# Performance work log

Hardware: AMD Instinct MI355X
Metric: run time of the kernel (lower is better)

## Reference

```python
import jax, jax.numpy as jnp
import numpy as np
from jax import lax

D_MODEL = 1024
N_HEADS = 16
HEAD_DIM = D_MODEL // N_HEADS
B, S = 4, 2048
EPS = 1e-5


def setup_inputs() -> dict:
    key = jax.random.key(0)
    ks = jax.random.split(key, 8)
    sc = 1.0 / np.sqrt(D_MODEL)
    return {
        "x": jax.random.normal(ks[0], (B, S, D_MODEL), dtype=jnp.float32),
        "Wq": jax.random.normal(ks[1], (D_MODEL, D_MODEL), dtype=jnp.float32) * sc,
        "Wk": jax.random.normal(ks[2], (D_MODEL, D_MODEL), dtype=jnp.float32) * sc,
        "Wv": jax.random.normal(ks[3], (D_MODEL, D_MODEL), dtype=jnp.float32) * sc,
        "Wa": jax.random.normal(ks[4], (D_MODEL, N_HEADS), dtype=jnp.float32) * sc,
        "ba": jnp.zeros((N_HEADS,), dtype=jnp.float32),
        "Wb": jax.random.normal(ks[5], (D_MODEL, N_HEADS), dtype=jnp.float32) * sc,
        "bb": jnp.zeros((N_HEADS,), dtype=jnp.float32),
        "Wg": jax.random.normal(ks[6], (D_MODEL, D_MODEL), dtype=jnp.float32) * sc,
        "Wo": jax.random.normal(ks[7], (D_MODEL, D_MODEL), dtype=jnp.float32) * sc,
        "g_norm": jnp.ones((D_MODEL,), dtype=jnp.float32),
    }


def _l2_normalize(v, eps=1e-12):
    # F.normalize(dim=-1) in float32
    v32 = v.astype(jnp.float32)
    n = jnp.sqrt(jnp.sum(v32 * v32, axis=-1, keepdims=True))
    return (v32 / jnp.maximum(n, eps)).astype(v.dtype)


def _rmsnorm(x, w):
    x32 = x.astype(jnp.float32)
    rms = lax.rsqrt(jnp.mean(x32 * x32, axis=-1, keepdims=True) + EPS)
    return (x32 * rms).astype(x.dtype) * w


def reference(x, Wq, Wk, Wv, Wa, ba, Wb, bb, Wg, Wo, g_norm):
    batch, seq_len, d_model = x.shape
    H, hd = N_HEADS, HEAD_DIM
    residual_input = x

    # projections -> [B, S, H, hd]
    q = (x @ Wq).reshape(batch, seq_len, H, hd)
    k = (x @ Wk).reshape(batch, seq_len, H, hd)
    v = (x @ Wv).reshape(batch, seq_len, H, hd)
    q = _l2_normalize(q)
    k = _l2_normalize(k)

    alpha = jax.nn.sigmoid(x @ Wa + ba)  # [B, S, H]
    beta = jax.nn.sigmoid(x @ Wb + bb)   # [B, S, H]

    # time-major for scan: [S, B, H, ...]
    qt = jnp.moveaxis(q, 1, 0)
    kt = jnp.moveaxis(k, 1, 0)
    vt = jnp.moveaxis(v, 1, 0)
    at = jnp.moveaxis(alpha, 1, 0)
    bt = jnp.moveaxis(beta, 1, 0)

    state0 = jnp.zeros((batch, H, hd, hd), dtype=x.dtype)

    def step(state, inp):
        q_t, k_t, v_t, a_t, b_t = inp  # [B,H,hd], [B,H]
        pred = jnp.einsum('bhde,bhd->bhe', state, k_t)
        error = v_t - pred
        update = jnp.einsum('bhe,bhd->bhde', b_t[..., None] * error, k_t)
        state = a_t[..., None, None] * state + update
        out = jnp.einsum('bhde,bhd->bhe', state, q_t)
        return state, out

    _, ys = lax.scan(step, state0, (qt, kt, vt, at, bt))  # ys: [S,B,H,hd]
    y = jnp.moveaxis(ys, 0, 1).reshape(batch, seq_len, d_model)

    gate = jax.nn.silu(residual_input @ Wg)
    y = _rmsnorm(y, g_norm) * gate
    return y @ Wo


if __name__ == "__main__":
    out = reference(**setup_inputs())
    print(out.shape)
```

## Files before the change

### kernel.cpp

```cpp
#include <hip/hip_runtime.h>
#include <hip/hip_bf16.h>
#include <math.h>

typedef __attribute__((ext_vector_type(8))) short bf16x8s;
typedef __attribute__((ext_vector_type(4))) float f32x4;

#define SEQ 2048
#define NTOK 8192
#define NQKV 3200

static __device__ __forceinline__ float bf2f(unsigned short u) {
  union { unsigned int i; float f; } c; c.i = ((unsigned int)u) << 16; return c.f;
}
static __device__ __forceinline__ unsigned short f2bf(float f) {
  union { float f; unsigned int i; } c; c.f = f;
  unsigned int x = c.i;
  return (unsigned short)((x + 0x7FFFu + ((x >> 16) & 1u)) >> 16);
}

static __device__ __forceinline__ float red16(float x) {
  union { float f; int i; } c, d;
  c.f = x; d.i = __builtin_amdgcn_update_dpp(0, c.i, 0xB1, 0xF, 0xF, true); x += d.f;
  c.f = x; d.i = __builtin_amdgcn_update_dpp(0, c.i, 0x4E, 0xF, 0xF, true); x += d.f;
  c.f = x; d.i = __builtin_amdgcn_update_dpp(0, c.i, 0x141, 0xF, 0xF, true); x += d.f;
  c.f = x; d.i = __builtin_amdgcn_update_dpp(0, c.i, 0x140, 0xF, 0xF, true); x += d.f;
  return x;
}

__global__ __launch_bounds__(256) void castx_k(const float* __restrict__ in,
                                               unsigned short* __restrict__ out, int n4) {
  int i = blockIdx.x * 256 + threadIdx.x;
  if (i >= n4) return;
  float4 v = ((const float4*)in)[i];
  ushort4 o;
  o.x = f2bf(v.x); o.y = f2bf(v.y); o.z = f2bf(v.z); o.w = f2bf(v.w);
  ((ushort4*)out)[i] = o;
}

__global__ void transpose_k(const float* __restrict__ in,
                            unsigned short* __restrict__ out, int R, int C) {
  __shared__ unsigned short tile[32][33];
  int c0 = blockIdx.x * 32, r0 = blockIdx.y * 32;
  int tx = threadIdx.x, ty = threadIdx.y;
  for (int i = ty; i < 32; i += 8)
    tile[i][tx] = f2bf(in[(size_t)(r0 + i) * C + c0 + tx]);
  __syncthreads();
  for (int i = ty; i < 32; i += 8)
    out[(size_t)(c0 + i) * R + r0 + tx] = tile[tx][i];
}

__global__ void build_wabT(const float* __restrict__ Wa,
                           const float* __restrict__ Wb,
                           unsigned short* __restrict__ rows) {
  int i = blockIdx.x * 256 + threadIdx.x;
  int j = i >> 10, k = i & 1023;
  float v = 0.f;
  if (j < 16) v = Wa[k * 16 + j];
  else if (j < 32) v = Wb[k * 16 + (j - 16)];
  rows[(size_t)j * 1024 + k] = f2bf(v);
}

template<int MODE>
__global__ __launch_bounds__(256) void gemm_bt(const unsigned short* __restrict__ A,
                                               const unsigned short* __restrict__ Bt,
                                               void* __restrict__ Cv,
                                               int M, int N, int K,
                                               const float* __restrict__ ba,
                                               const float* __restrict__ bbp,
                                               float* __restrict__ alphaF,
                                               float* __restrict__ betaF) {
  __shared__ __align__(16) unsigned short As[128 * 32];
  __shared__ __align__(16) unsigned short Bs[128 * 32];
  int tiles_n = N >> 7;
  int tm = blockIdx.x / tiles_n, tn = blockIdx.x % tiles_n;
  int m0 = tm << 7, n0 = tn << 7;
  int tid = threadIdx.x;
  int wave = tid >> 6, lane = tid & 63;
  int wm = wave >> 1, wn = wave & 1;
  int r = lane & 15, qd = lane >> 4;
  int lr = lane >> 2, lc = lane & 3;

  f32x4 acc[4][4];
#pragma unroll
  for (int mi = 0; mi < 4; mi++)
#pragma unroll
    for (int ni = 0; ni < 4; ni++) acc[mi][ni] = (f32x4){0.f, 0.f, 0.f, 0.f};

  for (int k0 = 0; k0 < K; k0 += 32) {
#pragma unroll
    for (int gi = 0; gi < 2; ++gi) {
      int g = wave + gi * 4;
      int row = g * 16 + lr;
      const unsigned short* ga = A + (size_t)(m0 + row) * K + k0 + lc * 8;
      const unsigned short* gb = Bt + (size_t)(n0 + row) * K + k0 + lc * 8;
      __builtin_amdgcn_global_load_lds(
          (const __attribute__((address_space(1))) unsigned int*)ga,
          (__attribute__((address_space(3))) unsigned int*)(As + g * 512 + lane * 8),
          16, 0, 0);
      __builtin_amdgcn_global_load_lds(
          (const __attribute__((address_space(1))) unsigned int*)gb,
          (__attribute__((address_space(3))) unsigned int*)(Bs + g * 512 + lane * 8),
          16, 0, 0);
    }
    __syncthreads();
    bf16x8s af[4], bfr[4];
#pragma unroll
    for (int mi = 0; mi < 4; mi++)
      af[mi] = *(const bf16x8s*)&As[(wm * 64 + mi * 16 + r) * 32 + qd * 8];
#pragma unroll
    for (int ni = 0; ni < 4; ni++)
      bfr[ni] = *(const bf16x8s*)&Bs[(wn * 64 + ni * 16 + r) * 32 + qd * 8];
#pragma unroll
    for (int mi = 0; mi < 4; mi++)
#pragma unroll
      for (int ni = 0; ni < 4; ni++)
        acc[mi][ni] = __builtin_amdgcn_mfma_f32_16x16x32_bf16(af[mi], bfr[ni], acc[mi][ni], 0, 0, 0);
    __syncthreads();
  }

  bool qk = (MODE == 2) && (n0 < 2048);
#pragma unroll
  for (int mi = 0; mi < 4; mi++) {
    f32x4 sc = (f32x4){1.f, 1.f, 1.f, 1.f};
    if (qk) {
      f32x4 ss = acc[mi][0] * acc[mi][0] + acc[mi][1] * acc[mi][1]
               + acc[mi][2] * acc[mi][2] + acc[mi][3] * acc[mi][3];
#pragma unroll
      for (int cc = 0; cc < 4; cc++) {
        float s = red16(ss[cc]);
        sc[cc] = 1.f / fmaxf(sqrtf(s), 1e-12f);
      }
    }
#pragma unroll
    for (int ni = 0; ni < 4; ni++)
#pragma unroll
      for (int reg = 0; reg < 4; reg++) {
        int m = m0 + wm * 64 + mi * 16 + qd * 4 + reg;
        int n = n0 + wn * 64 + ni * 16 + r;
        float a = acc[mi][ni][reg];
        if (MODE == 0) ((unsigned short*)Cv)[(size_t)m * N + n] = f2bf(a);
        else if (MODE == 1) ((float*)Cv)[(size_t)m * N + n] = a;
        else {
          if (qk) a *= sc[reg];
          if (n < 3072) ((unsigned short*)Cv)[(size_t)m * 3072 + n] = f2bf(a);
          else if (n < 3104) {
            int j = n - 3072;
            float bias = (j < 16) ? ba[j] : bbp[j - 16];
            float s = 1.f / (1.f + expf(-(a + bias)));
            if (j < 16) alphaF[(size_t)m * 16 + j] = s;
            else        betaF[(size_t)m * 16 + (j - 16)] = s;
          }
        }
      }
  }
}

#define D_OFF_STHI 0
#define D_OFF_STLO 8192
#define D_OFF_K    16384
#define D_OFF_Q    24576
#define D_OFF_V    32768
#define D_OFF_KT   40960
#define D_OFF_MT   45056
#define D_OFF_GBF  53248
#define D_OFF_CTHI 57344
#define D_OFF_CTLO 67584
#define D_OFF_W    77824
#define D_OFF_U    86016
#define D_OFF_AB   102400
#define D_LDS_SIZE 104512

static __device__ __forceinline__ float rdlane(float v, int i) {
  return __int_as_float(__builtin_amdgcn_readlane(__float_as_int(v), i));
}

__global__ __launch_bounds__(512, 2) void dscan_k(const unsigned short* __restrict__ qkv,
                                                  const float* __restrict__ alphaF,
                                                  const float* __restrict__ betaF,
                                                  unsigned short* __restrict__ y) {
  extern __shared__ char smem[];
  const int bh = blockIdx.x;
  const int b = bh >> 4, h = bh & 15;
  const int tid = threadIdx.x, wid = tid >> 6, lane = tid & 63;
  const int r = lane & 15, qd = lane >> 4;

  float* abf = (float*)(smem + D_OFF_AB);

  auto stage_jobs = [&](int cn) {
    int buf = cn & 1;
    int tok0 = b * SEQ + cn * 32;
    int row = lane >> 3, s8 = lane & 7;
    int sx = ((s8 ^ (row & 7)) * 8);
    {
      int p = (wid < 4) ? wid : wid - 4;
      int colbase = (wid < 4) ? (1024 + h * 64) : (h * 64);
      int off = (wid < 4) ? D_OFF_K : D_OFF_Q;
      const unsigned short* src = qkv + (size_t)(tok0 + p * 8 + row) * 3072 + colbase + sx;
      unsigned short* dst = (unsigned short*)(smem + off + buf * 4096 + p * 1024) + lane * 8;
      __builtin_amdgcn_global_load_lds(
          (const __attribute__((address_space(1))) unsigned int*)src,
          (__attribute__((address_space(3))) unsigned int*)dst, 16, 0, 0);
    }
    if (wid < 4) {
      int p = wid;
      const unsigned short* src = qkv + (size_t)(tok0 + p * 8 + row) * 3072 + 2048 + h * 64 + sx;
      unsigned short* dst = (unsigned short*)(smem + D_OFF_V + buf * 4096 + p * 1024) + lane * 8;
      __builtin_amdgcn_global_load_lds(
          (const __attribute__((address_space(1))) unsigned int*)src,
          (__attribute__((address_space(3))) unsigned int*)dst, 16, 0, 0);
    }
  };

  auto ab_compute = [&](int cn) {
    int t = lane & 31;
    int tok = b * SEQ + cn * 32 + t;
    float av = alphaF[(size_t)tok * 16 + h];
    float bv = betaF[(size_t)tok * 16 + h];
    float p = av;
#pragma unroll
    for (int s = 1; s < 32; s <<= 1) {
      float o = __shfl_up(p, s, 32);
      if ((lane & 31) >= s) p *= o;
    }
    float ep = __shfl_up(p, 1, 32);
    if ((lane & 31) == 0) ep = 1.f;
    float* ap = abf + (cn & 3) * 132;
    if (lane < 32) {
      ap[0 + t] = ep;
      ap[32 + t] = p;
      ap[64 + t] = 1.0f / p;
      if (t == 31) ap[128] = p;
    } else {
      ap[96 + t] = bv;
    }
  };

  auto gram_do = [&](int cn) {
    if (wid < 3 || wid > 6) return;
    int buf = cn & 1;
    const char* Kn = smem + D_OFF_K + buf * 4096;
    const char* Qn = smem + D_OFF_Q + buf * 4096;
    const float* ap = abf + (cn & 3) * 132;
    bool kk = (wid <= 4);
    int g0 = (kk ? (wid - 3) : (wid - 5)) * 2;
#pragma unroll
    for (int j = 0; j < 2; ++j) {
      int g = g0 + j, gi = g >> 1, gt = g & 1;
      f32x4 acc = (f32x4){0.f, 0.f, 0.f, 0.f};
#pragma unroll
      for (int ks = 0; ks < 2; ++ks) {
        int o = ks * 64 + qd * 16;
        bf16x8s af = *(const bf16x8s*)(Kn + (gi * 16 + r) * 128 + (o ^ ((r & 7) << 4)));
        bf16x8s bf = kk
            ? *(const bf16x8s*)(Kn + (gt * 16 + r) * 128 + (o ^ ((r & 7) << 4)))
            : *(const bf16x8s*)(Qn + (gt * 16 + r) * 128 + (o ^ ((r & 7) << 4)));
        acc = __builtin_amdgcn_mfma_f32_16x16x32_bf16(af, bf, acc, 0, 0, 0);
      }
      int tl = gt * 16 + r;
      f32x4 ei4 = *(const f32x4*)&ap[64 + gi * 16 + qd * 4];
      if (kk) {
        float bt = ap[96 + tl], ept = ap[0 + tl];
        float* Mtp = (float*)(smem + D_OFF_MT + buf * 4096);
#pragma unroll
        for (int reg = 0; reg < 4; ++reg) {
          int i = gi * 16 + qd * 4 + reg;
          Mtp[i * 32 + tl] = (i < tl) ? bt * ept * ei4[reg] * acc[reg] : 0.f;
        }
      } else {
        float et = ap[32 + tl];
        unsigned short* Gp = (unsigned short*)(smem + D_OFF_GBF + buf * 2048);
#pragma unroll
        for (int reg = 0; reg < 4; ++reg) {
          int i = gi * 16 + qd * 4 + reg;
          float v = (i <= tl) ? et * ei4[reg] * acc[reg] : 0.f;
          Gp[tl * 32 + i] = f2bf(v);
        }
      }
    }
  };

  float sreg[8];
#pragma unroll
  for (int i = 0; i < 8; ++i) sreg[i] = 0.f;

  {
    uint4 z = (uint4){0u, 0u, 0u, 0u};
    *(uint4*)(smem + D_OFF_STHI + tid * 16) = z;
    *(uint4*)(smem + D_OFF_STLO + tid * 16) = z;
  }
  stage_jobs(0);
  if (wid == 0) ab_compute(0);
  else if (wid == 1) ab_compute(1);
  __syncthreads();
  gram_do(0);
  __syncthreads();

  const char* SThi = smem + D_OFF_STHI;
  const char* STlo = smem + D_OFF_STLO;

  for (int c = 0; c < 64; ++c) {
    const int cbuf = c & 1, cs = c & 3;
    if (c + 1 < 64) stage_jobs(c + 1);
    {
      int tt = wid >> 2, te = wid & 3;
      const char* Kc = smem + D_OFF_K + cbuf * 4096;
      f32x4 acc = (f32x4){0.f, 0.f, 0.f, 0.f};
#pragma unroll
      for (int ks = 0; ks < 2; ++ks) {
        int o = ks * 64 + qd * 16;
        bf16x8s af = *(const bf16x8s*)(Kc + (tt * 16 + r) * 128 + (o ^ ((r & 7) << 4)));
        bf16x8s bhv = *(const bf16x8s*)(SThi + (te * 16 + r) * 128 + (o ^ ((r & 7) << 4)));
        bf16x8s blv = *(const bf16x8s*)(STlo + (te * 16 + r) * 128 + (o ^ ((r & 7) << 4)));
        acc = __builtin_amdgcn_mfma_f32_16x16x32_bf16(af, bhv, acc, 0, 0, 0);
        acc = __builtin_amdgcn_mfma_f32_16x16x32_bf16(af, blv, acc, 0, 0, 0);
      }
      float* Wp = (float*)(smem + D_OFF_W);
#pragma unroll
      for (int reg = 0; reg < 4; ++reg)
        Wp[(tt * 16 + qd * 4 + reg) * 64 + te * 16 + r] = acc[reg];
    }
    if (c >= 1) {
      int cc = c - 1, buf = cc & 1;
      int ty = wid >> 2, te = wid & 3;
      const char* Gp = smem + D_OFF_GBF + buf * 2048;
      bf16x8s af = *(const bf16x8s*)(Gp + (ty * 16 + r) * 64 + qd * 16);
      bf16x8s bhv = *(const bf16x8s*)(smem + D_OFF_CTHI + buf * 5120 + (te * 16 + r) * 80 + qd * 16);
      bf16x8s blv = *(const bf16x8s*)(smem + D_OFF_CTLO + buf * 5120 + (te * 16 + r) * 80 + qd * 16);
      f32x4 acc = (f32x4){0.f, 0.f, 0.f, 0.f};
      acc = __builtin_amdgcn_mfma_f32_16x16x32_bf16(af, bhv, acc, 0, 0, 0);
      acc = __builtin_amdgcn_mfma_f32_16x16x32_bf16(af, blv, acc, 0, 0, 0);
      const float* Up = (const float*)(smem + D_OFF_U + buf * 8192);
      f32x4 e4 = *(const f32x4*)&abf[(cc & 3) * 132 + 32 + ty * 16 + qd * 4];
#pragma unroll
      for (int reg = 0; reg < 4; ++reg) {
        int t = ty * 16 + qd * 4 + reg, e = te * 16 + r;
        float yv = fmaf(e4[reg], Up[t * 64 + e], acc[reg]);
        y[(size_t)(b * SEQ + cc * 32 + t) * 1024 + h * 64 + e] = f2bf(yv);
      }
    }
    __syncthreads();

    if (wid == 0) {
      const float* Wp = (const float*)(smem + D_OFF_W);
      const char* Vb = smem + D_OFF_V + cbuf * 4096;
      const float* ap = abf + cs * 132;
      float vb = ap[96 + (lane & 31)];
      float vep = ap[0 + (lane & 31)];
      float d_[32], r_[32];
#pragma unroll
      for (int i = 0; i < 32; ++i) r_[i] = 0.f;
#pragma unroll
      for (int i = 0; i < 32; ++i) {
        float w = Wp[i * 64 + lane];
        unsigned short vx = *(const unsigned short*)(Vb + (i * 128 + ((lane * 2) ^ ((i & 7) << 4))));
        d_[i] = rdlane(vb, i) * fmaf(-rdlane(vep, i), w, bf2f(vx));
      }
      const float* Mtp = (const float*)(smem + D_OFF_MT + cbuf * 4096);
#pragma unroll
      for (int i = 0; i < 32; ++i) {
        float cv = d_[i] - r_[i];
        d_[i] = cv;
#pragma unroll
        for (int cb4 = 0; cb4 < 8; ++cb4) {
          if (cb4 * 4 + 3 > i) {
            f32x4 m4 = *(const f32x4*)&Mtp[i * 32 + cb4 * 4];
            r_[cb4 * 4 + 0] = fmaf(m4[0], cv, r_[cb4 * 4 + 0]);
            r_[cb4 * 4 + 1] = fmaf(m4[1], cv, r_[cb4 * 4 + 1]);
            r_[cb4 * 4 + 2] = fmaf(m4[2], cv, r_[cb4 * 4 + 2]);
            r_[cb4 * 4 + 3] = fmaf(m4[3], cv, r_[cb4 * 4 + 3]);
          }
        }
      }
      unsigned int ph[16], pl[16];
#pragma unroll
      for (int j = 0; j < 16; ++j) {
        unsigned short h0 = f2bf(d_[2 * j]), h1 = f2bf(d_[2 * j + 1]);
        ph[j] = (unsigned int)h0 | ((unsigned int)h1 << 16);
        float l0 = d_[2 * j] - bf2f(h0), l1 = d_[2 * j + 1] - bf2f(h1);
        pl[j] = (unsigned int)f2bf(l0) | ((unsigned int)f2bf(l1) << 16);
      }
      char* Ch = smem + D_OFF_CTHI + cbuf * 5120 + lane * 80;
      char* Cl = smem + D_OFF_CTLO + cbuf * 5120 + lane * 80;
#pragma unroll
      for (int k = 0; k < 4; ++k) {
        *(uint4*)(Ch + k * 16) = (uint4){ph[4 * k], ph[4 * k + 1], ph[4 * k + 2], ph[4 * k + 3]};
        *(uint4*)(Cl + k * 16) = (uint4){pl[4 * k], pl[4 * k + 1], pl[4 * k + 2], pl[4 * k + 3]};
      }
    } else {
      if (wid <= 4) {
        const char* Qc = smem + D_OFF_Q + cbuf * 4096;
        float* Up = (float*)(smem + D_OFF_U + cbuf * 8192);
#pragma unroll
        for (int j = 0; j < 2; ++j) {
          int u = (wid - 1) * 2 + j, tu = u >> 2, te = u & 3;
          f32x4 acc = (f32x4){0.f, 0.f, 0.f, 0.f};
#pragma unroll
          for (int ks = 0; ks < 2; ++ks) {
            int o = ks * 64 + qd * 16;
            bf16x8s af = *(const bf16x8s*)(Qc + (tu * 16 + r) * 128 + (o ^ ((r & 7) << 4)));
            bf16x8s bhv = *(const bf16x8s*)(SThi + (te * 16 + r) * 128 + (o ^ ((r & 7) << 4)));
            bf16x8s blv = *(const bf16x8s*)(STlo + (te * 16 + r) * 128 + (o ^ ((r & 7) << 4)));
            acc = __builtin_amdgcn_mfma_f32_16x16x32_bf16(af, bhv, acc, 0, 0, 0);
            acc = __builtin_amdgcn_mfma_f32_16x16x32_bf16(af, blv, acc, 0, 0, 0);
          }
#pragma unroll
          for (int reg = 0; reg < 4; ++reg)
            Up[(tu * 16 + qd * 4 + reg) * 64 + te * 16 + r] = acc[reg];
        }
      }
      if (c + 1 < 64) gram_do(c + 1);
      if (wid == 7) {
        const float* ap = abf + cs * 132;
        float vei = ap[64 + (lane & 31)];
        float e31 = ap[128];
        const char* Kc = smem + D_OFF_K + cbuf * 4096;
        unsigned short* KT = (unsigned short*)(smem + D_OFF_KT);
        unsigned int pk[16];
#pragma unroll
        for (int i = 0; i < 32; ++i) {
          unsigned short kv = *(const unsigned short*)(Kc + (i * 128 + ((lane * 2) ^ ((i & 7) << 4))));
          float f = bf2f(kv) * (e31 * rdlane(vei, i));
          unsigned short o = f2bf(f);
          if (i & 1) pk[i >> 1] |= ((unsigned int)o << 16);
          else       pk[i >> 1] = o;
        }
#pragma unroll
        for (int k = 0; k < 4; ++k)
          *(uint4*)((char*)KT + lane * 64 + k * 16) =
              (uint4){pk[4 * k], pk[4 * k + 1], pk[4 * k + 2], pk[4 * k + 3]};
      }
      if (wid == 2 && c + 2 < 64) ab_compute(c + 2);
    }
    __syncthreads();

    {
      float e31 = abf[cs * 132 + 128];
      const char* KT = smem + D_OFF_KT;
#pragma unroll
      for (int j = 0; j < 2; ++j) {
        int s = wid * 2 + j, td = s >> 2, te = s & 3;
        bf16x8s af = *(const bf16x8s*)(KT + (td * 16 + r) * 64 + qd * 16);
        bf16x8s bhv = *(const bf16x8s*)(smem + D_OFF_CTHI + cbuf * 5120 + (te * 16 + r) * 80 + qd * 16);
        bf16x8s blv = *(const bf16x8s*)(smem + D_OFF_CTLO + cbuf * 5120 + (te * 16 + r) * 80 + qd * 16);
        f32x4 acc = (f32x4){0.f, 0.f, 0.f, 0.f};
        acc = __builtin_amdgcn_mfma_f32_16x16x32_bf16(af, bhv, acc, 0, 0, 0);
        acc = __builtin_amdgcn_mfma_f32_16x16x32_bf16(af, blv, acc, 0, 0, 0);
#pragma unroll
        for (int reg = 0; reg < 4; ++reg) {
          int d = td * 16 + qd * 4 + reg, e = te * 16 + r;
          float sv = fmaf(e31, sreg[j * 4 + reg], acc[reg]);
          sreg[j * 4 + reg] = sv;
          unsigned short hi = f2bf(sv);
          float lo = sv - bf2f(hi);
          *(unsigned short*)(smem + D_OFF_STHI + e * 128 + ((d * 2) ^ ((e & 7) << 4))) = hi;
          *(unsigned short*)(smem + D_OFF_STLO + e * 128 + ((d * 2) ^ ((e & 7) << 4))) = f2bf(lo);
        }
      }
    }
    __syncthreads();
  }

  {
    int cc = 63, buf = cc & 1;
    int ty = wid >> 2, te = wid & 3;
    const char* Gp = smem + D_OFF_GBF + buf * 2048;
    bf16x8s af = *(const bf16x8s*)(Gp + (ty * 16 + r) * 64 + qd * 16);
    bf16x8s bhv = *(const bf16x8s*)(smem + D_OFF_CTHI + buf * 5120 + (te * 16 + r) * 80 + qd * 16);
    bf16x8s blv = *(const bf16x8s*)(smem + D_OFF_CTLO + buf * 5120 + (te * 16 + r) * 80 + qd * 16);
    f32x4 acc = (f32x4){0.f, 0.f, 0.f, 0.f};
    acc = __builtin_amdgcn_mfma_f32_16x16x32_bf16(af, bhv, acc, 0, 0, 0);
    acc = __builtin_amdgcn_mfma_f32_16x16x32_bf16(af, blv, acc, 0, 0, 0);
    const float* Up = (const float*)(smem + D_OFF_U + buf * 8192);
    f32x4 e4 = *(const f32x4*)&abf[(cc & 3) * 132 + 32 + ty * 16 + qd * 4];
#pragma unroll
    for (int reg = 0; reg < 4; ++reg) {
      int t = ty * 16 + qd * 4 + reg, e = te * 16 + r;
      float yv = fmaf(e4[reg], Up[t * 64 + e], acc[reg]);
      y[(size_t)(b * SEQ + cc * 32 + t) * 1024 + h * 64 + e] = f2bf(yv);
    }
  }
}

__global__ __launch_bounds__(256) void rmsgate_k(const unsigned short* __restrict__ y,
                                                 const unsigned short* __restrict__ gl,
                                                 const float* __restrict__ gnorm,
                                                 unsigned short* __restrict__ z) {
  __shared__ float red[4];
  int row = blockIdx.x, tid = threadIdx.x;
  size_t base = (size_t)row * 1024 + tid * 4;
  uint2 yv = *(const uint2*)&y[base];
  float f0 = bf2f((unsigned short)(yv.x & 0xffff)), f1 = bf2f((unsigned short)(yv.x >> 16));
  float f2 = bf2f((unsigned short)(yv.y & 0xffff)), f3 = bf2f((unsigned short)(yv.y >> 16));
  float ss = f0 * f0 + f1 * f1 + f2 * f2 + f3 * f3;
#pragma unroll
  for (int s = 1; s < 64; s <<= 1) ss += __shfl_xor(ss, s);
  if ((tid & 63) == 0) red[tid >> 6] = ss;
  __syncthreads();
  ss = red[0] + red[1] + red[2] + red[3];
  float rms = rsqrtf(ss * (1.0f / 1024.0f) + 1e-5f);
  uint2 gv = *(const uint2*)&gl[base];
  float4 gn = *(const float4*)&gnorm[tid * 4];
  float g[4] = {bf2f((unsigned short)(gv.x & 0xffff)), bf2f((unsigned short)(gv.x >> 16)),
                bf2f((unsigned short)(gv.y & 0xffff)), bf2f((unsigned short)(gv.y >> 16))};
  float gnv[4] = {gn.x, gn.y, gn.z, gn.w};
  float fv[4] = {f0, f1, f2, f3};
  unsigned short o[4];
#pragma unroll
  for (int jj = 0; jj < 4; jj++) {
    float gate = g[jj] / (1.f + expf(-g[jj]));
    o[jj] = f2bf(fv[jj] * rms * gnv[jj] * gate);
  }
  uint2 ov;
  ov.x = (unsigned int)o[0] | ((unsigned int)o[1] << 16);
  ov.y = (unsigned int)o[2] | ((unsigned int)o[3] << 16);
  *(uint2*)&z[base] = ov;
}

extern "C" void kernel_launch(void* const* d_in, const int* in_sizes, int n_in,
                              void* d_out, int out_size, void* d_ws, size_t ws_size,
                              hipStream_t stream) {
  const float* x     = (const float*)d_in[0];
  const float* Wq    = (const float*)d_in[1];
  const float* Wk    = (const float*)d_in[2];
  const float* Wv    = (const float*)d_in[3];
  const float* Wa    = (const float*)d_in[4];
  const float* ba    = (const float*)d_in[5];
  const float* Wb    = (const float*)d_in[6];
  const float* bb    = (const float*)d_in[7];
  const float* Wg    = (const float*)d_in[8];
  const float* Wo    = (const float*)d_in[9];
  const float* gnorm = (const float*)d_in[10];
  float* out = (float*)d_out;

  unsigned short* xbf    = (unsigned short*)d_ws;
  unsigned short* Bt_qkv = xbf + (size_t)NTOK * 1024;
  unsigned short* Bt_g   = Bt_qkv + (size_t)NQKV * 1024;
  unsigned short* Bt_o   = Bt_g + (size_t)1024 * 1024;
  unsigned short* qkv    = Bt_o + (size_t)1024 * 1024;
  unsigned short* gatelin= qkv + (size_t)NTOK * 3072;
  unsigned short* ybuf   = gatelin + (size_t)NTOK * 1024;
  float* alphaF          = (float*)(ybuf + (size_t)NTOK * 1024);
  float* betaF           = alphaF + (size_t)NTOK * 16;
  unsigned short* zbuf   = xbf;

  static int dscan_inited = 0;
  if (!dscan_inited) {
    hipFuncSetAttribute((const void*)dscan_k,
                        hipFuncAttributeMaxDynamicSharedMemorySize, D_LDS_SIZE);
    dscan_inited = 1;
  }

  castx_k<<<NTOK * 1024 / 4 / 256, 256, 0, stream>>>(x, xbf, NTOK * 1024 / 4);
  dim3 tb(32, 8);
  transpose_k<<<dim3(32, 32), tb, 0, stream>>>(Wq, Bt_qkv, 1024, 1024);
  transpose_k<<<dim3(32, 32), tb, 0, stream>>>(Wk, Bt_qkv + (size_t)1024 * 1024, 1024, 1024);
  transpose_k<<<dim3(32, 32), tb, 0, stream>>>(Wv, Bt_qkv + (size_t)2048 * 1024, 1024, 1024);
  transpose_k<<<dim3(32, 32), tb, 0, stream>>>(Wg, Bt_g, 1024, 1024);
  transpose_k<<<dim3(32, 32), tb, 0, stream>>>(Wo, Bt_o, 1024, 1024);
  build_wabT<<<512, 256, 0, stream>>>(Wa, Wb, Bt_qkv + (size_t)3072 * 1024);

  gemm_bt<2><<<(NTOK / 128) * (NQKV / 128), 256, 0, stream>>>(
      xbf, Bt_qkv, qkv, NTOK, NQKV, 1024, ba, bb, alphaF, betaF);
  gemm_bt<0><<<(NTOK / 128) * (1024 / 128), 256, 0, stream>>>(
      xbf, Bt_g, gatelin, NTOK, 1024, 1024, nullptr, nullptr, nullptr, nullptr);
  dscan_k<<<64, 512, D_LDS_SIZE, stream>>>(qkv, alphaF, betaF, ybuf);
  rmsgate_k<<<NTOK, 256, 0, stream>>>(ybuf, gatelin, gnorm, zbuf);
  gemm_bt<1><<<(NTOK / 128) * (1024 / 128), 256, 0, stream>>>(
      zbuf, Bt_o, out, NTOK, 1024, 1024, nullptr, nullptr, nullptr, nullptr);
}
```

Measured before the change: 538.3 us.

## Reschedule delta-scan chunk pipeline: fuse W/U MFMAs, deepen prefetch, pad LDS

After: 1.567 ms. 2.91x slower.

```diff
diff --git a/kernel.cpp b/kernel.cpp
--- a/kernel.cpp
+++ b/kernel.cpp
@@ -155,20 +155,20 @@
   }
 }
 
-#define D_OFF_STHI 0
-#define D_OFF_STLO 8192
-#define D_OFF_K    16384
-#define D_OFF_Q    24576
-#define D_OFF_V    32768
-#define D_OFF_KT   40960
-#define D_OFF_MT   45056
-#define D_OFF_GBF  53248
-#define D_OFF_CTHI 57344
-#define D_OFF_CTLO 67584
-#define D_OFF_W    77824
-#define D_OFF_U    86016
-#define D_OFF_AB   102400
-#define D_LDS_SIZE 104512
+#define L_ST_HI 0
+#define L_ST_LO 8192
+#define L_K     16384
+#define L_Q     24576
+#define L_V     32768
+#define L_KT    45056
+#define L_MT    50176
+#define L_G     59392
+#define L_CTHI  65792
+#define L_CTLO  76032
+#define L_W     86272
+#define L_U     94720
+#define L_AB    111616
+#define L_SIZE  113792
 
 static __device__ __forceinline__ float rdlane(float v, int i) {
   return __int_as_float(__builtin_amdgcn_readlane(__float_as_int(v), i));
@@ -184,30 +184,33 @@
   const int tid = threadIdx.x, wid = tid >> 6, lane = tid & 63;
   const int r = lane & 15, qd = lane >> 4;
 
-  float* abf = (float*)(smem + D_OFF_AB);
-
-  auto stage_jobs = [&](int cn) {
-    int buf = cn & 1;
+  float* abf = (float*)(smem + L_AB);
+
+  auto stage_issue = [&](int cn) {
+    int bk = cn & 1, bv3 = cn % 3;
     int tok0 = b * SEQ + cn * 32;
     int row = lane >> 3, s8 = lane & 7;
     int sx = ((s8 ^ (row & 7)) * 8);
-    {
-      int p = (wid < 4) ? wid : wid - 4;
-      int colbase = (wid < 4) ? (1024 + h * 64) : (h * 64);
-      int off = (wid < 4) ? D_OFF_K : D_OFF_Q;
-      const unsigned short* src = qkv + (size_t)(tok0 + p * 8 + row) * 3072 + colbase + sx;
-      unsigned short* dst = (unsigned short*)(smem + off + buf * 4096 + p * 1024) + lane * 8;
+    if (wid >= 1 && wid <= 4) {
+      int p = wid - 1;
+      const unsigned short* srck = qkv + (size_t)(tok0 + p * 8 + row) * 3072 + 1024 + h * 64 + sx;
+      unsigned short* dstk = (unsigned short*)(smem + L_K + bk * 4096 + p * 1024) + lane * 8;
       __builtin_amdgcn_global_load_lds(
-          (const __attribute__((address_space(1))) unsigned int*)src,
-          (__attribute__((address_space(3))) unsigned int*)dst, 16, 0, 0);
-    }
-    if (wid < 4) {
-      int p = wid;
-      const unsigned short* src = qkv + (size_t)(tok0 + p * 8 + row) * 3072 + 2048 + h * 64 + sx;
-      unsigned short* dst = (unsigned short*)(smem + D_OFF_V + buf * 4096 + p * 1024) + lane * 8;
+          (const __attribute__((address_space(1))) unsigned int*)srck,
+          (__attribute__((address_space(3))) unsigned int*)dstk, 16, 0, 0);
+      const unsigned short* srcv = qkv + (size_t)(tok0 + p * 8 + row) * 3072 + 2048 + h * 64 + sx;
+      unsigned short* dstv = (unsigned short*)(smem + L_V + bv3 * 4096 + p * 1024) + lane * 8;
       __builtin_amdgcn_global_load_lds(
-          (const __attribute__((address_space(1))) unsigned int*)src,
-          (__attribute__((address_space(3))) unsigned int*)dst, 16, 0, 0);
+          (const __attribute__((address_space(1))) unsigned int*)srcv,
+          (__attribute__((address_space(3))) unsigned int*)dstv, 16, 0, 0);
+    }
+    if (wid >= 4) {
+      int p = (wid == 4) ? 3 : (wid - 5);
+      const unsigned short* srcq = qkv + (size_t)(tok0 + p * 8 + row) * 3072 + h * 64 + sx;
+      unsigned short* dstq = (unsigned short*)(smem + L_Q + bk * 4096 + p * 1024) + lane * 8;
+      __builtin_amdgcn_global_load_lds(
+          (const __attribute__((address_space(1))) unsigned int*)srcq,
+          (__attribute__((address_space(3))) unsigned int*)dstq, 16, 0, 0);
     }
   };
 
@@ -224,7 +227,7 @@
     }
     float ep = __shfl_up(p, 1, 32);
     if ((lane & 31) == 0) ep = 1.f;
-    float* ap = abf + (cn & 3) * 132;
+    float* ap = abf + (cn & 3) * 136;
     if (lane < 32) {
       ap[0 + t] = ep;
       ap[32 + t] = p;
@@ -238,9 +241,9 @@
   auto gram_do = [&](int cn) {
     if (wid < 3 || wid > 6) return;
     int buf = cn & 1;
-    const char* Kn = smem + D_OFF_K + buf * 4096;
-    const char* Qn = smem + D_OFF_Q + buf * 4096;
-    const float* ap = abf + (cn & 3) * 132;
+    const char* Kn = smem + L_K + buf * 4096;
+    const char* Qn = smem + L_Q + buf * 4096;
+    const float* ap = abf + (cn & 3) * 136;
     bool kk = (wid <= 4);
     int g0 = (kk ? (wid - 3) : (wid - 5)) * 2;
 #pragma unroll
@@ -260,21 +263,47 @@
       f32x4 ei4 = *(const f32x4*)&ap[64 + gi * 16 + qd * 4];
       if (kk) {
         float bt = ap[96 + tl], ept = ap[0 + tl];
-        float* Mtp = (float*)(smem + D_OFF_MT + buf * 4096);
+        float* Mtp = (float*)(smem + L_MT + buf * 4608);
 #pragma unroll
         for (int reg = 0; reg < 4; ++reg) {
           int i = gi * 16 + qd * 4 + reg;
-          Mtp[i * 32 + tl] = (i < tl) ? bt * ept * ei4[reg] * acc[reg] : 0.f;
+          Mtp[i * 36 + tl] = (i < tl) ? bt * ept * ei4[reg] * acc[reg] : 0.f;
         }
       } else {
         float et = ap[32 + tl];
-        unsigned short* Gp = (unsigned short*)(smem + D_OFF_GBF + buf * 2048);
+        unsigned short* Gp = (unsigned short*)(smem + L_G + buf * 3200);
 #pragma unroll
         for (int reg = 0; reg < 4; ++reg) {
           int i = gi * 16 + qd * 4 + reg;
           float v = (i <= tl) ? et * ei4[reg] * acc[reg] : 0.f;
-          Gp[tl * 32 + i] = f2bf(v);
+          Gp[tl * 40 + i] = f2bf(v);
         }
+      }
+    }
+  };
+
+  auto y_do = [&](int cc) {
+    if (wid < 2 || wid > 5) return;
+    int buf = cc & 1;
+    const char* Gp = smem + L_G + buf * 3200;
+    const float* Up = (const float*)(smem + L_U + buf * 8448);
+    const float* ap = abf + (cc & 3) * 136;
+#pragma unroll
+    for (int j = 0; j < 2; ++j) {
+      int idx = (wid - 2) * 2 + j;
+      int ty = idx >> 2, te = idx & 3;
+      bf16x8s af = *(const bf16x8s*)(Gp + (ty * 16 + r) * 80 + qd * 16);
+      bf16x8s bhv = *(const bf16x8s*)(smem + L_CTHI + buf * 5120 + (te * 16 + r) * 80 + qd * 16);
+      bf16x8s blv = *(const bf16x8s*)(smem + L_CTLO + buf * 5120 + (te * 16 + r) * 80 + qd * 16);
+      f32x4 acc = (f32x4){0.f, 0.f, 0.f, 0.f};
+      acc = __builtin_amdgcn_mfma_f32_16x16x32_bf16(af, bhv, acc, 0, 0, 0);
+      acc = __builtin_amdgcn_mfma_f32_16x16x32_bf16(af, blv, acc, 0, 0, 0);
+      f32x4 e4 = *(const f32x4*)&ap[32 + ty * 16 + qd * 4];
+#pragma unroll
+      for (int reg = 0; reg < 4; ++reg) {
+        int t = ty * 16 + qd * 4 + reg, e = te * 16 + r;
+        float yv = fmaf(e4[reg], Up[t * 66 + e], acc[reg]);
+        y[(size_t)(b * SEQ + cc * 32 + t) * 1024 + h * 64 + e] = f2bf(yv);
       }
     }
   };
@@ -285,65 +314,76 @@
 
   {
     uint4 z = (uint4){0u, 0u, 0u, 0u};
-    *(uint4*)(smem + D_OFF_STHI + tid * 16) = z;
-    *(uint4*)(smem + D_OFF_STLO + tid * 16) = z;
+    *(uint4*)(smem + L_ST_HI + tid * 16) = z;
+    *(uint4*)(smem + L_ST_LO + tid * 16) = z;
   }
-  stage_jobs(0);
+  stage_issue(0);
+  stage_issue(1);
   if (wid == 0) ab_compute(0);
   else if (wid == 1) ab_compute(1);
   __syncthreads();
   gram_do(0);
   __syncthreads();
 
-  const char* SThi = smem + D_OFF_STHI;
-  const char* STlo = smem + D_OFF_STLO;
+  const char* SThi = smem + L_ST_HI;
+  const char* STlo = smem + L_ST_LO;
 
   for (int c = 0; c < 64; ++c) {
     const int cbuf = c & 1, cs = c & 3;
-    if (c + 1 < 64) stage_jobs(c + 1);
     {
       int tt = wid >> 2, te = wid & 3;
-      const char* Kc = smem + D_OFF_K + cbuf * 4096;
-      f32x4 acc = (f32x4){0.f, 0.f, 0.f, 0.f};
+      const char* Kc = smem + L_K + cbuf * 4096;
+      const char* Qc = smem + L_Q + cbuf * 4096;
+      f32x4 accw = (f32x4){0.f, 0.f, 0.f, 0.f};
+      f32x4 accu = (f32x4){0.f, 0.f, 0.f, 0.f};
 #pragma unroll
       for (int ks = 0; ks < 2; ++ks) {
         int o = ks * 64 + qd * 16;
-        bf16x8s af = *(const bf16x8s*)(Kc + (tt * 16 + r) * 128 + (o ^ ((r & 7) << 4)));
         bf16x8s bhv = *(const bf16x8s*)(SThi + (te * 16 + r) * 128 + (o ^ ((r & 7) << 4)));
         bf16x8s blv = *(const bf16x8s*)(STlo + (te * 16 + r) * 128 + (o ^ ((r & 7) << 4)));
-        acc = __builtin_amdgcn_mfma_f32_16x16x32_bf16(af, bhv, acc, 0, 0, 0);
-        acc = __builtin_amdgcn_mfma_f32_16x16x32_bf16(af, blv, acc, 0, 0, 0);
-      }
-      float* Wp = (float*)(smem + D_OFF_W);
-#pragma unroll
-      for (int reg = 0; reg < 4; ++reg)
-        Wp[(tt * 16 + qd * 4 + reg) * 64 + te * 16 + r] = acc[reg];
-    }
-    if (c >= 1) {
-      int cc = c - 1, buf = cc & 1;
-      int ty = wid >> 2, te = wid & 3;
-      const char* Gp = smem + D_OFF_GBF + buf * 2048;
-      bf16x8s af = *(const bf16x8s*)(Gp + (ty * 16 + r) * 64 + qd * 16);
-      bf16x8s bhv = *(const bf16x8s*)(smem + D_OFF_CTHI + buf * 5120 + (te * 16 + r) * 80 + qd * 16);
-      bf16x8s blv = *(const bf16x8s*)(smem + D_OFF_CTLO + buf * 5120 + (te * 16 + r) * 80 + qd * 16);
-      f32x4 acc = (f32x4){0.f, 0.f, 0.f, 0.f};
-      acc = __builtin_amdgcn_mfma_f32_16x16x32_bf16(af, bhv, acc, 0, 0, 0);
-      acc = __builtin_amdgcn_mfma_f32_16x16x32_bf16(af, blv, acc, 0, 0, 0);
-      const float* Up = (const float*)(smem + D_OFF_U + buf * 8192);
-      f32x4 e4 = *(const f32x4*)&abf[(cc & 3) * 132 + 32 + ty * 16 + qd * 4];
+        bf16x8s afk = *(const bf16x8s*)(Kc + (tt * 16 + r) * 128 + (o ^ ((r & 7) << 4)));
+        bf16x8s afq = *(const bf16x8s*)(Qc + (tt * 16 + r) * 128 + (o ^ ((r & 7) << 4)));
+        accw = __builtin_amdgcn_mfma_f32_16x16x32_bf16(afk, bhv, accw, 0, 0, 0);
+        accw = __builtin_amdgcn_mfma_f32_16x16x32_bf16(afk, blv, accw, 0, 0, 0);
+        accu = __builtin_amdgcn_mfma_f32_16x16x32_bf16(afq, bhv, accu, 0, 0, 0);
+        accu = __builtin_amdgcn_mfma_f32_16x16x32_bf16(afq, blv, accu, 0, 0, 0);
+      }
+      float* Wp = (float*)(smem + L_W);
+      float* Up = (float*)(smem + L_U + cbuf * 8448);
 #pragma unroll
       for (int reg = 0; reg < 4; ++reg) {
-        int t = ty * 16 + qd * 4 + reg, e = te * 16 + r;
-        float yv = fmaf(e4[reg], Up[t * 64 + e], acc[reg]);
-        y[(size_t)(b * SEQ + cc * 32 + t) * 1024 + h * 64 + e] = f2bf(yv);
-      }
+        Wp[(tt * 16 + qd * 4 + reg) * 66 + te * 16 + r] = accw[reg];
+        Up[(tt * 16 + qd * 4 + reg) * 66 + te * 16 + r] = accu[reg];
+      }
+    }
+    if (wid == 5 || wid == 6) {
+      const float* ap = abf + cs * 136;
+      float vei = ap[64 + (lane & 31)];
+      float e31 = ap[128];
+      const char* Kc = smem + L_K + cbuf * 4096;
+      int i0 = (wid - 5) * 16;
+      unsigned int pk[8];
+#pragma unroll
+      for (int ii = 0; ii < 16; ++ii) {
+        int i = i0 + ii;
+        unsigned short kv = *(const unsigned short*)(Kc + (i * 128 + ((lane * 2) ^ ((i & 7) << 4))));
+        float f = bf2f(kv) * (e31 * rdlane(vei, i));
+        unsigned short o = f2bf(f);
+        if (ii & 1) pk[ii >> 1] |= ((unsigned int)o << 16);
+        else        pk[ii >> 1] = o;
+      }
+      char* KTp = smem + L_KT + lane * 80 + i0 * 2;
+      *(uint4*)(KTp)      = (uint4){pk[0], pk[1], pk[2], pk[3]};
+      *(uint4*)(KTp + 16) = (uint4){pk[4], pk[5], pk[6], pk[7]};
     }
     __syncthreads();
 
+    if (c + 2 < 64) stage_issue(c + 2);
     if (wid == 0) {
-      const float* Wp = (const float*)(smem + D_OFF_W);
-      const char* Vb = smem + D_OFF_V + cbuf * 4096;
-      const float* ap = abf + cs * 132;
+      __builtin_amdgcn_s_setprio(1);
+      const float* Wp = (const float*)(smem + L_W);
+      const char* Vb = smem + L_V + (c % 3) * 4096;
+      const float* ap = abf + cs * 136;
       float vb = ap[96 + (lane & 31)];
       float vep = ap[0 + (lane & 31)];
       float d_[32], r_[32];
@@ -351,11 +391,11 @@
       for (int i = 0; i < 32; ++i) r_[i] = 0.f;
 #pragma unroll
       for (int i = 0; i < 32; ++i) {
-        float w = Wp[i * 64 + lane];
+        float w = Wp[i * 66 + lane];
         unsigned short vx = *(const unsigned short*)(Vb + (i * 128 + ((lane * 2) ^ ((i & 7) << 4))));
         d_[i] = rdlane(vb, i) * fmaf(-rdlane(vep, i), w, bf2f(vx));
       }
-      const float* Mtp = (const float*)(smem + D_OFF_MT + cbuf * 4096);
+      const float* Mtp = (const float*)(smem + L_MT + cbuf * 4608);
 #pragma unroll
       for (int i = 0; i < 32; ++i) {
         float cv = d_[i] - r_[i];
@@ -363,7 +403,7 @@
 #pragma unroll
         for (int cb4 = 0; cb4 < 8; ++cb4) {
           if (cb4 * 4 + 3 > i) {
-            f32x4 m4 = *(const f32x4*)&Mtp[i * 32 + cb4 * 4];
+            f32x4 m4 = *(const f32x4*)&Mtp[i * 36 + cb4 * 4];
             r_[cb4 * 4 + 0] = fmaf(m4[0], cv, r_[cb4 * 4 + 0]);
             r_[cb4 * 4 + 1] = fmaf(m4[1], cv, r_[cb4 * 4 + 1]);
             r_[cb4 * 4 + 2] = fmaf(m4[2], cv, r_[cb4 * 4 + 2]);
@@ -371,6 +411,7 @@
           }
         }
       }
+      __builtin_amdgcn_s_setprio(0);
       unsigned int ph[16], pl[16];
 #pragma unroll
       for (int j = 0; j < 16; ++j) {
@@ -379,69 +420,27 @@
         float l0 = d_[2 * j] - bf2f(h0), l1 = d_[2 * j + 1] - bf2f(h1);
         pl[j] = (unsigned int)f2bf(l0) | ((unsigned int)f2bf(l1) << 16);
       }
-      char* Ch = smem + D_OFF_CTHI + cbuf * 5120 + lane * 80;
-      char* Cl = smem + D_OFF_CTLO + cbuf * 5120 + lane * 80;
+      char* Ch = smem + L_CTHI + cbuf * 5120 + lane * 80;
+      char* Cl = smem + L_CTLO + cbuf * 5120 + lane * 80;
 #pragma unroll
       for (int k = 0; k < 4; ++k) {
         *(uint4*)(Ch + k * 16) = (uint4){ph[4 * k], ph[4 * k + 1], ph[4 * k + 2], ph[4 * k + 3]};
         *(uint4*)(Cl + k * 16) = (uint4){pl[4 * k], pl[4 * k + 1], pl[4 * k + 2], pl[4 * k + 3]};
       }
-    } else {
-      if (wid <= 4) {
-        const char* Qc = smem + D_OFF_Q + cbuf * 4096;
-        float* Up = (float*)(smem + D_OFF_U + cbuf * 8192);
-#pragma unroll
-        for (int j = 0; j < 2; ++j) {
-          int u = (wid - 1) * 2 + j, tu = u >> 2, te = u & 3;
-          f32x4 acc = (f32x4){0.f, 0.f, 0.f, 0.f};
-#pragma unroll
-          for (int ks = 0; ks < 2; ++ks) {
-            int o = ks * 64 + qd * 16;
-            bf16x8s af = *(const bf16x8s*)(Qc + (tu * 16 + r) * 128 + (o ^ ((r & 7) << 4)));
-            bf16x8s bhv = *(const bf16x8s*)(SThi + (te * 16 + r) * 128 + (o ^ ((r & 7) << 4)));
-            bf16x8s blv = *(const bf16x8s*)(STlo + (te * 16 + r) * 128 + (o ^ ((r & 7) << 4)));
-            acc = __builtin_amdgcn_mfma_f32_16x16x32_bf16(af, bhv, acc, 0, 0, 0);
-            acc = __builtin_amdgcn_mfma_f32_16x16x32_bf16(af, blv, acc, 0, 0, 0);
-          }
-#pragma unroll
-          for (int reg = 0; reg < 4; ++reg)
-            Up[(tu * 16 + qd * 4 + reg) * 64 + te * 16 + r] = acc[reg];
-        }
-      }
-      if (c + 1 < 64) gram_do(c + 1);
-      if (wid == 7) {
-        const float* ap = abf + cs * 132;
-        float vei = ap[64 + (lane & 31)];
-        float e31 = ap[128];
-        const char* Kc = smem + D_OFF_K + cbuf * 4096;
-        unsigned short* KT = (unsigned short*)(smem + D_OFF_KT);
-        unsigned int pk[16];
-#pragma unroll
-        for (int i = 0; i < 32; ++i) {
-          unsigned short kv = *(const unsigned short*)(Kc + (i * 128 + ((lane * 2) ^ ((i & 7) << 4))));
-          float f = bf2f(kv) * (e31 * rdlane(vei, i));
-          unsigned short o = f2bf(f);
-          if (i & 1) pk[i >> 1] |= ((unsigned int)o << 16);
-          else       pk[i >> 1] = o;
-        }
-#pragma unroll
-        for (int k = 0; k < 4; ++k)
-          *(uint4*)((char*)KT + lane * 64 + k * 16) =
-              (uint4){pk[4 * k], pk[4 * k + 1], pk[4 * k + 2], pk[4 * k + 3]};
-      }
-      if (wid == 2 && c + 2 < 64) ab_compute(c + 2);
-    }
+    }
+    if (wid == 1 && c + 2 < 64) ab_compute(c + 2);
+    if (c >= 1) y_do(c - 1);
     __syncthreads();
 
     {
-      float e31 = abf[cs * 132 + 128];
-      const char* KT = smem + D_OFF_KT;
+      float e31 = abf[cs * 136 + 128];
+      const char* KT = smem + L_KT;
 #pragma unroll
       for (int j = 0; j < 2; ++j) {
         int s = wid * 2 + j, td = s >> 2, te = s & 3;
-        bf16x8s af = *(const bf16x8s*)(KT + (td * 16 + r) * 64 + qd * 16);
-        bf16x8s bhv = *(const bf16x8s*)(smem + D_OFF_CTHI + cbuf * 5120 + (te * 16 + r) * 80 + qd * 16);
-        bf16x8s blv = *(const bf16x8s*)(smem + D_OFF_CTLO + cbuf * 5120 + (te * 16 + r) * 80 + qd * 16);
+        bf16x8s af = *(const bf16x8s*)(KT + (td * 16 + r) * 80 + qd * 16);
+        bf16x8s bhv = *(const bf16x8s*)(smem + L_CTHI + cbuf * 5120 + (te * 16 + r) * 80 + qd * 16);
+        bf16x8s blv = *(const bf16x8s*)(smem + L_CTLO + cbuf * 5120 + (te * 16 + r) * 80 + qd * 16);
         f32x4 acc = (f32x4){0.f, 0.f, 0.f, 0.f};
         acc = __builtin_amdgcn_mfma_f32_16x16x32_bf16(af, bhv, acc, 0, 0, 0);
         acc = __builtin_amdgcn_mfma_f32_16x16x32_bf16(af, blv, acc, 0, 0, 0);
@@ -452,33 +451,16 @@
           sreg[j * 4 + reg] = sv;
           unsigned short hi = f2bf(sv);
           float lo = sv - bf2f(hi);
-          *(unsigned short*)(smem + D_OFF_STHI + e * 128 + ((d * 2) ^ ((e & 7) << 4))) = hi;
-          *(unsigned short*)(smem + D_OFF_STLO + e * 128 + ((d * 2) ^ ((e & 7) << 4))) = f2bf(lo);
+          *(unsigned short*)(smem + L_ST_HI + e * 128 + ((d * 2) ^ ((e & 7) << 4))) = hi;
+          *(unsigned short*)(smem + L_ST_LO + e * 128 + ((d * 2) ^ ((e & 7) << 4))) = f2bf(lo);
         }
       }
     }
+    if (c + 1 < 64) gram_do(c + 1);
     __syncthreads();
   }
 
-  {
-    int cc = 63, buf = cc & 1;
-    int ty = wid >> 2, te = wid & 3;
-    const char* Gp = smem + D_OFF_GBF + buf * 2048;
-    bf16x8s af = *(const bf16x8s*)(Gp + (ty * 16 + r) * 64 + qd * 16);
-    bf16x8s bhv = *(const bf16x8s*)(smem + D_OFF_CTHI + buf * 5120 + (te * 16 + r) * 80 + qd * 16);
-    bf16x8s blv = *(const bf16x8s*)(smem + D_OFF_CTLO + buf * 5120 + (te * 16 + r) * 80 + qd * 16);
-    f32x4 acc = (f32x4){0.f, 0.f, 0.f, 0.f};
-    acc = __builtin_amdgcn_mfma_f32_16x16x32_bf16(af, bhv, acc, 0, 0, 0);
-    acc = __builtin_amdgcn_mfma_f32_16x16x32_bf16(af, blv, acc, 0, 0, 0);
-    const float* Up = (const float*)(smem + D_OFF_U + buf * 8192);
-    f32x4 e4 = *(const f32x4*)&abf[(cc & 3) * 132 + 32 + ty * 16 + qd * 4];
-#pragma unroll
-    for (int reg = 0; reg < 4; ++reg) {
-      int t = ty * 16 + qd * 4 + reg, e = te * 16 + r;
-      float yv = fmaf(e4[reg], Up[t * 64 + e], acc[reg]);
-      y[(size_t)(b * SEQ + cc * 32 + t) * 1024 + h * 64 + e] = f2bf(yv);
-    }
-  }
+  y_do(63);
 }
 
 __global__ __launch_bounds__(256) void rmsgate_k(const unsigned short* __restrict__ y,
@@ -546,7 +528,7 @@
   static int dscan_inited = 0;
   if (!dscan_inited) {
     hipFuncSetAttribute((const void*)dscan_k,
-                        hipFuncAttributeMaxDynamicSharedMemorySize, D_LDS_SIZE);
+                        hipFuncAttributeMaxDynamicSharedMemorySize, L_SIZE);
     dscan_inited = 1;
   }
 
@@ -563,7 +545,7 @@
       xbf, Bt_qkv, qkv, NTOK, NQKV, 1024, ba, bb, alphaF, betaF);
   gemm_bt<0><<<(NTOK / 128) * (1024 / 128), 256, 0, stream>>>(
       xbf, Bt_g, gatelin, NTOK, 1024, 1024, nullptr, nullptr, nullptr, nullptr);
-  dscan_k<<<64, 512, D_LDS_SIZE, stream>>>(qkv, alphaF, betaF, ybuf);
+  dscan_k<<<64, 512, L_SIZE, stream>>>(qkv, alphaF, betaF, ybuf);
   rmsgate_k<<<NTOK, 256, 0, stream>>>(ybuf, gatelin, gnorm, zbuf);
   gemm_bt<1><<<(NTOK / 128) * (1024 / 128), 256, 0, stream>>>(
       zbuf, Bt_o, out, NTOK, 1024, 1024, nullptr, nullptr, nullptr, nullptr);
```
